# Kernel optimization log

Measured on AMD Instinct MI355X. Metric: run time of the kernel, lower is better.

The kernel has to match this reference:

```python
import jax, jax.numpy as jnp
import numpy as np

B, S, D = 4, 2048, 1152
H, KVH, HD = 16, 4, 64
SW = 1792
NEG = jnp.float32(-1e9)


def setup_inputs() -> dict:
    key = jax.random.key(0)
    ks = jax.random.split(key, 6)
    x = jax.random.normal(ks[0], (B, S, D), jnp.float32)
    s = 0.02
    wq = jax.random.normal(ks[1], (H * HD, D), jnp.float32) * s
    wk = jax.random.normal(ks[2], (KVH * HD, D), jnp.float32) * s
    wv = jax.random.normal(ks[3], (KVH * HD, D), jnp.float32) * s
    wo = jax.random.normal(ks[4], (D, H * HD), jnp.float32) * s
    # rotary freqs: theta=10000, standard llama-style
    inv = 1.0 / (10000.0 ** (np.arange(0, HD, 2, dtype=np.float32) / HD))
    t = np.arange(S, dtype=np.float32)
    fr = np.outer(t, inv)  # [S, HD//2]
    freqs_cos = jnp.asarray(np.cos(fr), jnp.float32)
    freqs_sin = jnp.asarray(np.sin(fr), jnp.float32)
    positions = jnp.arange(S, dtype=jnp.int32)
    # sliding-window causal additive mask: attend j iff 0 <= i-j < SW
    i = jnp.arange(S)[:, None]
    j = jnp.arange(S)[None, :]
    allowed = (j <= i) & (i - j < SW)
    mask = jnp.where(allowed, jnp.float32(0.0), NEG)
    cache_k = jnp.zeros((B, SW, KVH, HD), jnp.float32)
    cache_v = jnp.zeros((B, SW, KVH, HD), jnp.float32)
    return {"x": x, "wq": wq, "wk": wk, "wv": wv, "wo": wo,
            "freqs_cos": freqs_cos, "freqs_sin": freqs_sin, "mask": mask,
            "cache_k": cache_k, "cache_v": cache_v, "positions": positions}


def _rope(t, cos, sin):
    # t: [B,S,h,HD]; complex multiply on (even, odd) pairs
    tr = t.reshape(t.shape[:-1] + (HD // 2, 2))
    a, b = tr[..., 0], tr[..., 1]
    c = cos[None, :, None, :]
    s = sin[None, :, None, :]
    out = jnp.stack([a * c - b * s, a * s + b * c], axis=-1)
    return out.reshape(t.shape)


def reference(x, wq, wk, wv, wo, freqs_cos, freqs_sin, mask, cache_k, cache_v, positions):
    bsz, seqlen, _ = x.shape
    xq = jnp.einsum('bsd,ed->bse', x, wq).reshape(bsz, seqlen, H, HD)
    xk = jnp.einsum('bsd,ed->bse', x, wk).reshape(bsz, seqlen, KVH, HD)
    xv = jnp.einsum('bsd,ed->bse', x, wv).reshape(bsz, seqlen, KVH, HD)
    xq = _rope(xq, freqs_cos, freqs_sin)
    xk = _rope(xk, freqs_cos, freqs_sin)
    # circular-buffer cache scatter (last SW tokens, modulo indexing)
    idx = positions[-SW:] % SW
    new_ck = cache_k.at[:, idx].set(xk[:, -SW:])
    new_cv = cache_v.at[:, idx].set(xv[:, -SW:])
    # GQA: expand kv heads (repeat_interleave on head dim)
    rep = H // KVH
    key = jnp.repeat(xk, rep, axis=2)   # [B,S,H,HD]
    value = jnp.repeat(xv, rep, axis=2)
    q = xq.transpose(0, 2, 1, 3)        # [B,H,S,HD]
    k = key.transpose(0, 2, 1, 3)
    v = value.transpose(0, 2, 1, 3)
    scale = 1.0 / jnp.sqrt(jnp.float32(HD))
    scores = jnp.einsum('bhqd,bhkd->bhqk', q, k) * scale + mask[None, None]
    probs = jax.nn.softmax(scores, axis=-1)
    out = jnp.einsum('bhqk,bhkd->bhqd', probs, v)
    out = out.transpose(0, 2, 1, 3).reshape(bsz, seqlen, H * HD)
    out = jnp.einsum('bse,de->bsd', out, wo)
    return out, new_ck, new_cv
```

## Files before the change

### kernel.cpp

```cpp
#include <hip/hip_runtime.h>
#include <cstdint>
#include <cstddef>


typedef unsigned short u16;
typedef unsigned int   u32;
typedef __attribute__((ext_vector_type(8))) short bf16x8;
typedef __attribute__((ext_vector_type(4))) float f32x4;

#define AS1(p) ((const __attribute__((address_space(1))) void*)(p))
#define AS3(p) ((__attribute__((address_space(3))) void*)(p))

__device__ __forceinline__ u16 f2bf(float f) {
  u32 u = __float_as_uint(f);
  u += 0x7fffu + ((u >> 16) & 1u);
  return (u16)(u >> 16);
}
__device__ __forceinline__ float bf2f(u32 x) { return __uint_as_float(x << 16); }
__device__ __forceinline__ f32x4 mfma16(bf16x8 a, bf16x8 b, f32x4 c) {
  return __builtin_amdgcn_mfma_f32_16x16x32_bf16(a, b, c, 0, 0, 0);
}
__device__ __forceinline__ u32 cvtpk_bf16(float lo, float hi) {
  u32 r;
  asm("v_cvt_pk_bf16_f32 %0, %1, %2" : "=v"(r) : "v"(lo), "v"(hi));
  return r;
}

__global__ __launch_bounds__(256) void cvt5_kernel(const float* __restrict__ x,
                                                   const float* __restrict__ wq,
                                                   const float* __restrict__ wk,
                                                   const float* __restrict__ wv,
                                                   const float* __restrict__ wo,
                                                   u16* __restrict__ xb,
                                                   u16* __restrict__ wqkvb,
                                                   u16* __restrict__ wob) {
  int i = blockIdx.x * 256 + threadIdx.x;
  const float* in; u16* out; int off;
  if (i < 2359296)      { in = x;  out = xb;                  off = i; }
  else if (i < 2654208) { in = wq; out = wqkvb;               off = i - 2359296; }
  else if (i < 2727936) { in = wk; out = wqkvb + 1024 * 1152; off = i - 2654208; }
  else if (i < 2801664) { in = wv; out = wqkvb + 1280 * 1152; off = i - 2727936; }
  else                  { in = wo; out = wob;                 off = i - 2801664; }
  float4 v = ((const float4*)in)[off];
  uint2 o;
  o.x = (u32)f2bf(v.x) | ((u32)f2bf(v.y) << 16);
  o.y = (u32)f2bf(v.z) | ((u32)f2bf(v.w) << 16);
  ((uint2*)out)[off] = o;
}

template<int BF16_OUT>
__global__ __launch_bounds__(256) void gemm_bt(const u16* __restrict__ A,
                                               const u16* __restrict__ B,
                                               void* __restrict__ C,
                                               int M, int N, int K, int NT) {
  __shared__ u16 As[128][64];
  __shared__ u16 Bs[128][64];
  const int tid  = threadIdx.x;
  const int w    = tid >> 6, lane = tid & 63;
  const int l15  = lane & 15, hi4 = lane >> 4;
  const int lid  = blockIdx.x;
  const int k_   = lid >> 3;
  const int by   = (lid & 7) + 8 * (k_ / NT);
  const int bx   = k_ % NT;
  const int m0   = by * 128, n0 = bx * 128;
  const int wr   = w >> 1, wc = w & 1;

  const int srow = lane >> 3;
  const int scol = ((lane & 7) ^ srow) << 3;
  const u16* Ab = A + (size_t)(m0 + w * 32 + srow) * K + scol;
  const u16* Bb = B + (size_t)(n0 + w * 32 + srow) * K + scol;
  u16* AsDst = &As[w * 32][0];
  u16* BsDst = &Bs[w * 32][0];

  const int swz = (l15 & 7) << 4;
  const int c0  = (((hi4 * 16)      ^ swz) >> 1);
  const int c1  = (((64 + hi4 * 16) ^ swz) >> 1);
  const u16* aRd = &As[wr * 64 + l15][0];
  const u16* bRd = &Bs[wc * 64 + l15][0];

  f32x4 acc[4][4] = {};

  for (int kk = 0; kk < K; kk += 64) {
#pragma unroll
    for (int q = 0; q < 4; q++) {
      __builtin_amdgcn_global_load_lds(AS1(Ab + kk + (size_t)q * 8 * K),
                                       AS3(AsDst + q * 8 * 64), 16, 0, 0);
      __builtin_amdgcn_global_load_lds(AS1(Bb + kk + (size_t)q * 8 * K),
                                       AS3(BsDst + q * 8 * 64), 16, 0, 0);
    }
    __syncthreads();
#pragma unroll
    for (int ks = 0; ks < 2; ks++) {
      const int cc = ks ? c1 : c0;
      bf16x8 af[4], bfr[4];
#pragma unroll
      for (int t = 0; t < 4; t++) af[t]  = *(const bf16x8*)(aRd + t * 16 * 64 + cc);
#pragma unroll
      for (int t = 0; t < 4; t++) bfr[t] = *(const bf16x8*)(bRd + t * 16 * 64 + cc);
#pragma unroll
      for (int mi = 0; mi < 4; mi++)
#pragma unroll
        for (int ni = 0; ni < 4; ni++)
          acc[mi][ni] = mfma16(af[mi], bfr[ni], acc[mi][ni]);
    }
    __syncthreads();
  }

#pragma unroll
  for (int mi = 0; mi < 4; mi++) {
#pragma unroll
    for (int r = 0; r < 4; r++) {
      int row = m0 + wr * 64 + mi * 16 + hi4 * 4 + r;
      size_t base = (size_t)row * N + n0 + wc * 64 + l15;
#pragma unroll
      for (int ni = 0; ni < 4; ni++) {
        float v = acc[mi][ni][r];
        if (BF16_OUT) ((u16*)C)[base + ni * 16] = f2bf(v);
        else          ((float*)C)[base + ni * 16] = v;
      }
    }
  }
}

__global__ __launch_bounds__(256) void ropev_kernel(u16* __restrict__ buf,
                                                    float* __restrict__ kcache,
                                                    u16* __restrict__ vT,
                                                    float* __restrict__ ncv,
                                                    const float* __restrict__ cosT,
                                                    const float* __restrict__ sinT) {
  __shared__ u16 tile[64][65];
  if (blockIdx.x < 20480) {
    int idx = blockIdx.x * 256 + threadIdx.x;
    const bool isQ = idx < 4194304;
    int pi = isQ ? idx : idx - 4194304;
    int m  = isQ ? (pi >> 9) : (pi >> 7);
    int p  = isQ ? (pi & 511) : (pi & 127);
    int coloff = isQ ? 0 : 512;
    int s = m & 2047, b = m >> 11;
    int hh = p & 31;
    u32* bp = (u32*)buf + (size_t)m * 768 + coloff + p;
    u32 pk = *bp;
    float a  = bf2f(pk & 0xffffu), bb = bf2f(pk >> 16);
    float c  = cosT[s * 32 + hh],  sn = sinT[s * 32 + hh];
    float o0 = a * c - bb * sn;
    float o1 = a * sn + bb * c;
    const float qs = isQ ? 0.18033688011112042f : 1.0f;
    *bp = (u32)f2bf(o0 * qs) | ((u32)f2bf(o1 * qs) << 16);
    if (!isQ && s >= 256) {
      int pc = (s < 1792) ? s : s - 1792;
      float2* cp = (float2*)(kcache + (size_t)(b * 1792 + pc) * 256 + 2 * p);
      *cp = make_float2(o0, o1);
    }
  } else {
    int bi = blockIdx.x - 20480;
    int s0 = (bi & 31) * 64, kvh = (bi >> 5) & 3, b = bi >> 7;
    int t = threadIdx.x;
    int r = t >> 2, cc = (t & 3) * 16;
    const u16* src = buf + (size_t)(b * 2048 + s0 + r) * 1536 + 1280 + kvh * 64 + cc;
    uint4 v0 = *(const uint4*)src;
    uint4 v1 = *(const uint4*)(src + 8);
    u16 vals[16];
    *(uint4*)&vals[0] = v0;
    *(uint4*)&vals[8] = v1;
    int s = s0 + r;
    if (s >= 256) {
      int pc = (s < 1792) ? s : s - 1792;
      float* dst = ncv + (size_t)(b * 1792 + pc) * 256 + kvh * 64 + cc;
#pragma unroll
      for (int i = 0; i < 16; i += 4) {
        float4 f = make_float4(bf2f(vals[i]), bf2f(vals[i + 1]),
                               bf2f(vals[i + 2]), bf2f(vals[i + 3]));
        *(float4*)(dst + i) = f;
      }
    }
#pragma unroll
    for (int i = 0; i < 16; i++) tile[cc + i][r] = vals[i];
    __syncthreads();
    u16 ov[16];
#pragma unroll
    for (int i = 0; i < 16; i++) ov[i] = tile[r][cc + i];
    u16* dst2 = vT + (size_t)((b * 4 + kvh) * 64 + r) * 2048 + s0 + cc;
    *(uint4*)dst2 = *(uint4*)&ov[0];
    *(uint4*)(dst2 + 8) = *(uint4*)&ov[8];
  }
}

__global__ __launch_bounds__(256) void attn_kernel(const u16* __restrict__ qkv,
                                                   const u16* __restrict__ vT,
                                                   u16* __restrict__ attnb) {
  __shared__ __align__(16) u16 Kbuf[2][64][64];
  __shared__ __align__(16) u16 Vbuf[2][64][64];
  const int tid = threadIdx.x;
  const int w = tid >> 6, lane = tid & 63;
  const int l15 = lane & 15, hi4 = lane >> 4;

  const int lid  = blockIdx.x;
  const int wgid = (lid & 7) * 128 + (lid >> 3);
  const int gx   = wgid & 63;
  const int rr   = wgid >> 6;
  const int kvh  = rr & 3, b = rr >> 2;
  const int i0   = 32 * (63 - gx);
  const int h    = kvh * 4 + w;

  const u16* qbase = qkv + (size_t)(b * 2048) * 1536 + h * 64;
  const u16* kbase = qkv + (size_t)(b * 2048) * 1536 + 1024 + kvh * 64;
  const u16* vbase = vT + (size_t)((b * 4 + kvh) * 64) * 2048;

  bf16x8 qa[2][2];
  {
    const u16* qp = qbase + (size_t)(i0 + l15) * 1536 + hi4 * 8;
#pragma unroll
    for (int m = 0; m < 2; m++)
#pragma unroll
      for (int ki = 0; ki < 2; ki++)
        qa[m][ki] = *(const bf16x8*)(qp + m * 16 * 1536 + ki * 32);
  }

  bf16x8 ones;
#pragma unroll
  for (int i = 0; i < 8; i++) ones[i] = (short)0x3F80;

  f32x4 o[2][4] = {};
  f32x4 ol[2] = {};

  const int srow = lane >> 3;
  const int ssl  = (lane & 7) ^ srow;

#define STAGE(J0, BS)                                                                     \
  do {                                                                                    \
    _Pragma("unroll")                                                                     \
    for (int q = 0; q < 2; q++) {                                                         \
      const int row = 32 * q + 8 * w + srow;                                              \
      __builtin_amdgcn_global_load_lds(AS1(kbase + (size_t)((J0) + row) * 1536 + ssl * 8),\
                                       AS3(&Kbuf[BS][32 * q + 8 * w][0]), 16, 0, 0);      \
      __builtin_amdgcn_global_load_lds(AS1(vbase + (size_t)row * 2048 + (J0) + ssl * 8),  \
                                       AS3(&Vbuf[BS][32 * q + 8 * w][0]), 16, 0, 0);      \
    }                                                                                     \
  } while (0)

  int jstart = i0 - 1791;
  if (jstart < 0) jstart = 0;
  jstart &= ~63;
  const int jend = i0 + 32;
  const int ntiles = (jend - jstart + 63) >> 6;

  STAGE(jstart, 0);
  if (ntiles > 1) STAGE(jstart + 64, 1);

  for (int t = 0; t < ntiles; t++) {
    const int j0 = jstart + 64 * t;
    if (t + 1 < ntiles) asm volatile("s_waitcnt vmcnt(4)" ::: "memory");
    else                asm volatile("s_waitcnt vmcnt(0)" ::: "memory");
    __builtin_amdgcn_s_barrier();
    __builtin_amdgcn_sched_barrier(0);

    const u16* Kb = &Kbuf[t & 1][0][0];
    const u16* Vb = &Vbuf[t & 1][0][0];

    bf16x8 kf[2][4];
#pragma unroll
    for (int nt = 0; nt < 4; nt++)
#pragma unroll
      for (int ki = 0; ki < 2; ki++)
        kf[ki][nt] = *(const bf16x8*)(Kb + (nt * 16 + l15) * 64 +
                                      (((ki * 4 + hi4) ^ (l15 & 7)) << 3));

    u32 vfd[4][2][4];
#pragma unroll
    for (int tt = 0; tt < 4; tt++) {
      const int row = tt * 16 + l15;
      const u16* Vrow = Vb + row * 64;
      const int rs = row & 7;
      const int inner = (hi4 & 1) * 4;
      const int h1 = hi4 >> 1;
#pragma unroll
      for (int kbp = 0; kbp < 2; kbp++) {
        int us0 = (((4 * kbp + h1)     ^ rs) << 3) + inner;
        int us1 = (((4 * kbp + 2 + h1) ^ rs) << 3) + inner;
        uint2 lo = *(const uint2*)(Vrow + us0);
        uint2 hi = *(const uint2*)(Vrow + us1);
        vfd[tt][kbp][0] = lo.x; vfd[tt][kbp][1] = lo.y;
        vfd[tt][kbp][2] = hi.x; vfd[tt][kbp][3] = hi.y;
      }
    }
    asm volatile("s_waitcnt lgkmcnt(0)" ::: "memory");
    __builtin_amdgcn_sched_barrier(0);
    __builtin_amdgcn_s_barrier();
    if (t + 2 < ntiles) STAGE(j0 + 128, t & 1);

    __builtin_amdgcn_s_setprio(1);
    const bool fast = (j0 + 63 <= i0) && (i0 + 31 - j0 < 1792);
#pragma unroll
    for (int m = 0; m < 2; m++) {
      __align__(16) u32 pkb[8];
#pragma unroll
      for (int nt = 0; nt < 4; nt++) {
        f32x4 s = {0.f, 0.f, 0.f, 0.f};
        s = mfma16(kf[0][nt], qa[m][0], s);
        s = mfma16(kf[1][nt], qa[m][1], s);
        float p[4];
        if (fast) {
#pragma unroll
          for (int r = 0; r < 4; r++) p[r] = __builtin_amdgcn_exp2f(s[r]);
        } else {
#pragma unroll
          for (int r = 0; r < 4; r++) {
            const int j = j0 + nt * 16 + hi4 * 4 + r;
            const int i = i0 + m * 16 + l15;
            p[r] = (j <= i && i - j < 1792) ? __builtin_amdgcn_exp2f(s[r]) : 0.f;
          }
        }
        pkb[nt * 2]     = cvtpk_bf16(p[0], p[1]);
        pkb[nt * 2 + 1] = cvtpk_bf16(p[2], p[3]);
      }
      bf16x8 pa0 = *(const bf16x8*)&pkb[0];
      bf16x8 pa1 = *(const bf16x8*)&pkb[4];
#pragma unroll
      for (int tt = 0; tt < 4; tt++) {
        o[m][tt] = mfma16(pa0, *(const bf16x8*)&vfd[tt][0][0], o[m][tt]);
        o[m][tt] = mfma16(pa1, *(const bf16x8*)&vfd[tt][1][0], o[m][tt]);
      }
      ol[m] = mfma16(pa0, ones, ol[m]);
      ol[m] = mfma16(pa1, ones, ol[m]);
    }
    __builtin_amdgcn_s_setprio(0);
  }
#undef STAGE

  u16* op = attnb + (size_t)(b * 2048 + i0 + hi4 * 4) * 1024 + h * 64 + l15;
#pragma unroll
  for (int m = 0; m < 2; m++)
#pragma unroll
    for (int r = 0; r < 4; r++) {
      float inv = 1.0f / ol[m][r];
#pragma unroll
      for (int tt = 0; tt < 4; tt++)
        op[(size_t)(m * 16 + r) * 1024 + 16 * tt] = f2bf(o[m][tt][r] * inv);
    }
}

extern "C" void kernel_launch(void* const* d_in, const int* in_sizes, int n_in,
                              void* d_out, int out_size, void* d_ws, size_t ws_size,
                              hipStream_t stream) {
  const float* x  = (const float*)d_in[0];
  const float* wq = (const float*)d_in[1];
  const float* wk = (const float*)d_in[2];
  const float* wv = (const float*)d_in[3];
  const float* wo = (const float*)d_in[4];
  const float* fc = (const float*)d_in[5];
  const float* fs = (const float*)d_in[6];

  float* out = (float*)d_out;
  float* nck = out + 9437184;
  float* ncv = nck + 1835008;

  char* ws = (char*)d_ws;
  u16* attnb = (u16*)(ws);
  u16* xb    = (u16*)(ws);
  u16* wqkvb = (u16*)(ws + 18874368);
  u16* wob   = (u16*)(ws + 22413312);
  u16* qkv   = (u16*)(ws + 24772608);
  u16* vT    = (u16*)(ws + 49938432);

  cvt5_kernel<<<12096, 256, 0, stream>>>(x, wq, wk, wv, wo, xb, wqkvb, wob);

  gemm_bt<1><<<768, 256, 0, stream>>>(xb, wqkvb, qkv, 8192, 1536, 1152, 12);

  ropev_kernel<<<20992, 256, 0, stream>>>(qkv, nck, vT, ncv, fc, fs);

  attn_kernel<<<1024, 256, 0, stream>>>(qkv, vT, attnb);

  gemm_bt<0><<<576, 256, 0, stream>>>(attnb, wob, out, 8192, 1152, 1024, 9);
}
```

Measured before the change: 161.3 us.

## Fuse Q rotary into attention Q load and fold softmax scale into Wq

Q rope is now applied in registers when the attention kernel loads its Q fragments, and the softmax scale is folded into the bf16 conversion of Wq. The separate rope kernel only processes K and the V transpose, which removes a full read-modify-write pass over Q. The attention workgroup-to-tile mapping is also changed to interleave long and short causal rows for load balance. Applying the scale before rounding slightly changes bf16 rounding.

```diff
diff --git a/kernel.cpp b/kernel.cpp
--- a/kernel.cpp
+++ b/kernel.cpp
@@ -35,16 +35,17 @@
                                                    u16* __restrict__ wqkvb,
                                                    u16* __restrict__ wob) {
   int i = blockIdx.x * 256 + threadIdx.x;
-  const float* in; u16* out; int off;
+  const float* in; u16* out; int off; float sc = 1.0f;
   if (i < 2359296)      { in = x;  out = xb;                  off = i; }
-  else if (i < 2654208) { in = wq; out = wqkvb;               off = i - 2359296; }
+  else if (i < 2654208) { in = wq; out = wqkvb;               off = i - 2359296;
+                          sc = 0.18033688011112042f; }
   else if (i < 2727936) { in = wk; out = wqkvb + 1024 * 1152; off = i - 2654208; }
   else if (i < 2801664) { in = wv; out = wqkvb + 1280 * 1152; off = i - 2727936; }
   else                  { in = wo; out = wob;                 off = i - 2801664; }
   float4 v = ((const float4*)in)[off];
   uint2 o;
-  o.x = (u32)f2bf(v.x) | ((u32)f2bf(v.y) << 16);
-  o.y = (u32)f2bf(v.z) | ((u32)f2bf(v.w) << 16);
+  o.x = (u32)f2bf(v.x * sc) | ((u32)f2bf(v.y * sc) << 16);
+  o.y = (u32)f2bf(v.z * sc) | ((u32)f2bf(v.w * sc) << 16);
   ((uint2*)out)[off] = o;
 }
 
@@ -129,30 +130,25 @@
                                                     const float* __restrict__ cosT,
                                                     const float* __restrict__ sinT) {
   __shared__ u16 tile[64][65];
-  if (blockIdx.x < 20480) {
+  if (blockIdx.x < 4096) {
     int idx = blockIdx.x * 256 + threadIdx.x;
-    const bool isQ = idx < 4194304;
-    int pi = isQ ? idx : idx - 4194304;
-    int m  = isQ ? (pi >> 9) : (pi >> 7);
-    int p  = isQ ? (pi & 511) : (pi & 127);
-    int coloff = isQ ? 0 : 512;
+    int m = idx >> 7, p = idx & 127;
     int s = m & 2047, b = m >> 11;
     int hh = p & 31;
-    u32* bp = (u32*)buf + (size_t)m * 768 + coloff + p;
+    u32* bp = (u32*)buf + (size_t)m * 768 + 512 + p;
     u32 pk = *bp;
     float a  = bf2f(pk & 0xffffu), bb = bf2f(pk >> 16);
     float c  = cosT[s * 32 + hh],  sn = sinT[s * 32 + hh];
     float o0 = a * c - bb * sn;
     float o1 = a * sn + bb * c;
-    const float qs = isQ ? 0.18033688011112042f : 1.0f;
-    *bp = (u32)f2bf(o0 * qs) | ((u32)f2bf(o1 * qs) << 16);
-    if (!isQ && s >= 256) {
+    *bp = (u32)f2bf(o0) | ((u32)f2bf(o1) << 16);
+    if (s >= 256) {
       int pc = (s < 1792) ? s : s - 1792;
       float2* cp = (float2*)(kcache + (size_t)(b * 1792 + pc) * 256 + 2 * p);
       *cp = make_float2(o0, o1);
     }
   } else {
-    int bi = blockIdx.x - 20480;
+    int bi = blockIdx.x - 4096;
     int s0 = (bi & 31) * 64, kvh = (bi >> 5) & 3, b = bi >> 7;
     int t = threadIdx.x;
     int r = t >> 2, cc = (t & 3) * 16;
@@ -187,20 +183,24 @@
 
 __global__ __launch_bounds__(256) void attn_kernel(const u16* __restrict__ qkv,
                                                    const u16* __restrict__ vT,
-                                                   u16* __restrict__ attnb) {
+                                                   u16* __restrict__ attnb,
+                                                   const float* __restrict__ cosT,
+                                                   const float* __restrict__ sinT) {
   __shared__ __align__(16) u16 Kbuf[2][64][64];
   __shared__ __align__(16) u16 Vbuf[2][64][64];
   const int tid = threadIdx.x;
   const int w = tid >> 6, lane = tid & 63;
   const int l15 = lane & 15, hi4 = lane >> 4;
 
-  const int lid  = blockIdx.x;
-  const int wgid = (lid & 7) * 128 + (lid >> 3);
-  const int gx   = wgid & 63;
-  const int rr   = wgid >> 6;
-  const int kvh  = rr & 3, b = rr >> 2;
-  const int i0   = 32 * (63 - gx);
-  const int h    = kvh * 4 + w;
+  const int lid = blockIdx.x;
+  const int g   = lid & 7;
+  const int t_  = lid >> 3;
+  const int u_  = t_ >> 1, v_ = t_ & 1;
+  const int c   = v_ ? u_ : (63 - u_);
+  const int rr  = 2 * g + v_;
+  const int kvh = rr & 3, b = rr >> 2;
+  const int i0  = 32 * c;
+  const int h   = kvh * 4 + w;
 
   const u16* qbase = qkv + (size_t)(b * 2048) * 1536 + h * 64;
   const u16* kbase = qkv + (size_t)(b * 2048) * 1536 + 1024 + kvh * 64;
@@ -210,10 +210,34 @@
   {
     const u16* qp = qbase + (size_t)(i0 + l15) * 1536 + hi4 * 8;
 #pragma unroll
-    for (int m = 0; m < 2; m++)
-#pragma unroll
-      for (int ki = 0; ki < 2; ki++)
-        qa[m][ki] = *(const bf16x8*)(qp + m * 16 * 1536 + ki * 32);
+    for (int m = 0; m < 2; m++) {
+      const int s = i0 + m * 16 + l15;
+#pragma unroll
+      for (int ki = 0; ki < 2; ki++) {
+        bf16x8 qv = *(const bf16x8*)(qp + m * 16 * 1536 + ki * 32);
+        const int hh0 = ki * 16 + hi4 * 4;
+        float4 cs = *(const float4*)(cosT + s * 32 + hh0);
+        float4 sn = *(const float4*)(sinT + s * 32 + hh0);
+        u32 wds[4];
+        {
+          float a = bf2f((u16)qv[0]), bb2 = bf2f((u16)qv[1]);
+          wds[0] = cvtpk_bf16(a * cs.x - bb2 * sn.x, a * sn.x + bb2 * cs.x);
+        }
+        {
+          float a = bf2f((u16)qv[2]), bb2 = bf2f((u16)qv[3]);
+          wds[1] = cvtpk_bf16(a * cs.y - bb2 * sn.y, a * sn.y + bb2 * cs.y);
+        }
+        {
+          float a = bf2f((u16)qv[4]), bb2 = bf2f((u16)qv[5]);
+          wds[2] = cvtpk_bf16(a * cs.z - bb2 * sn.z, a * sn.z + bb2 * cs.z);
+        }
+        {
+          float a = bf2f((u16)qv[6]), bb2 = bf2f((u16)qv[7]);
+          wds[3] = cvtpk_bf16(a * cs.w - bb2 * sn.w, a * sn.w + bb2 * cs.w);
+        }
+        qa[m][ki] = *(const bf16x8*)&wds[0];
+      }
+    }
   }
 
   bf16x8 ones;
@@ -366,9 +390,9 @@
 
   gemm_bt<1><<<768, 256, 0, stream>>>(xb, wqkvb, qkv, 8192, 1536, 1152, 12);
 
-  ropev_kernel<<<20992, 256, 0, stream>>>(qkv, nck, vT, ncv, fc, fs);
-
-  attn_kernel<<<1024, 256, 0, stream>>>(qkv, vT, attnb);
+  ropev_kernel<<<4608, 256, 0, stream>>>(qkv, nck, vT, ncv, fc, fs);
+
+  attn_kernel<<<1024, 256, 0, stream>>>(qkv, vT, attnb, fc, fs);
 
   gemm_bt<0><<<576, 256, 0, stream>>>(attnb, wob, out, 8192, 1152, 1024, 9);
 }
```

Result: slower. 183.8 us (+14.0%).

## Split long attention query tiles across two workgroups and merge partial results

Applied to the files above, without the earlier changes.

Query tiles in rows 1536-2047, which have the longest key ranges, are now split into two halves along the key dimension and handled by separate workgroups. Each half writes unnormalized fp32 partial outputs and row sums to workspace, and a new merge kernel adds them and normalizes. The grid grows from 1024 to 1280 blocks and is reordered to balance per-XCD load and shorten the tail. The cost is an extra kernel launch plus fp32 partial-result traffic. Summing un-rescaled partials is valid only because the kernel uses no running max.

```diff
diff --git a/kernel.cpp b/kernel.cpp
--- a/kernel.cpp
+++ b/kernel.cpp
@@ -187,20 +187,28 @@
 
 __global__ __launch_bounds__(256) void attn_kernel(const u16* __restrict__ qkv,
                                                    const u16* __restrict__ vT,
-                                                   u16* __restrict__ attnb) {
+                                                   u16* __restrict__ attnb,
+                                                   float* __restrict__ Opart,
+                                                   float* __restrict__ lpart) {
   __shared__ __align__(16) u16 Kbuf[2][64][64];
   __shared__ __align__(16) u16 Vbuf[2][64][64];
   const int tid = threadIdx.x;
   const int w = tid >> 6, lane = tid & 63;
   const int l15 = lane & 15, hi4 = lane >> 4;
 
-  const int lid  = blockIdx.x;
-  const int wgid = (lid & 7) * 128 + (lid >> 3);
-  const int gx   = wgid & 63;
-  const int rr   = wgid >> 6;
-  const int kvh  = rr & 3, b = rr >> 2;
-  const int i0   = 32 * (63 - gx);
-  const int h    = kvh * 4 + w;
+  const int lid   = blockIdx.x;
+  const int xcd   = lid & 7;
+  const int t_    = lid >> 3;
+  const int panel = (t_ >= 80) ? 1 : 0;
+  const int seq   = t_ - 80 * panel;
+  int c, half = 0, split = 0;
+  if (seq < 24)      { c = 47 - seq; }
+  else if (seq < 56) { int ci = seq - 24; c = 63 - (ci >> 1); half = ci & 1; split = 1; }
+  else               { c = 79 - seq; }
+  const int rr  = 2 * xcd + panel;
+  const int kvh = rr & 3, b = rr >> 2;
+  const int i0  = 32 * c;
+  const int h   = kvh * 4 + w;
 
   const u16* qbase = qkv + (size_t)(b * 2048) * 1536 + h * 64;
   const u16* kbase = qkv + (size_t)(b * 2048) * 1536 + 1024 + kvh * 64;
@@ -241,16 +249,21 @@
   int jstart = i0 - 1791;
   if (jstart < 0) jstart = 0;
   jstart &= ~63;
-  const int jend = i0 + 32;
-  const int ntiles = (jend - jstart + 63) >> 6;
-
-  STAGE(jstart, 0);
-  if (ntiles > 1) STAGE(jstart + 64, 1);
-
-  for (int t = 0; t < ntiles; t++) {
-    const int j0 = jstart + 64 * t;
-    if (t + 1 < ntiles) asm volatile("s_waitcnt vmcnt(4)" ::: "memory");
-    else                asm volatile("s_waitcnt vmcnt(0)" ::: "memory");
+  const int T = (i0 + 32 - jstart + 63) >> 6;
+  int js = jstart, ntc = T;
+  if (split) {
+    const int nF = (T + 1) >> 1;
+    if (half == 0) { ntc = nF; }
+    else           { js = jstart + 64 * nF; ntc = T - nF; }
+  }
+
+  STAGE(js, 0);
+  if (ntc > 1) STAGE(js + 64, 1);
+
+  for (int t = 0; t < ntc; t++) {
+    const int j0 = js + 64 * t;
+    if (t + 1 < ntc) asm volatile("s_waitcnt vmcnt(4)" ::: "memory");
+    else             asm volatile("s_waitcnt vmcnt(0)" ::: "memory");
     __builtin_amdgcn_s_barrier();
     __builtin_amdgcn_sched_barrier(0);
 
@@ -286,7 +299,7 @@
     asm volatile("s_waitcnt lgkmcnt(0)" ::: "memory");
     __builtin_amdgcn_sched_barrier(0);
     __builtin_amdgcn_s_barrier();
-    if (t + 2 < ntiles) STAGE(j0 + 128, t & 1);
+    if (t + 2 < ntc) STAGE(j0 + 128, t & 1);
 
     __builtin_amdgcn_s_setprio(1);
     const bool fast = (j0 + 63 <= i0) && (i0 + 31 - j0 < 1792);
@@ -327,16 +340,58 @@
   }
 #undef STAGE
 
-  u16* op = attnb + (size_t)(b * 2048 + i0 + hi4 * 4) * 1024 + h * 64 + l15;
-#pragma unroll
-  for (int m = 0; m < 2; m++)
-#pragma unroll
-    for (int r = 0; r < 4; r++) {
-      float inv = 1.0f / ol[m][r];
-#pragma unroll
-      for (int tt = 0; tt < 4; tt++)
-        op[(size_t)(m * 16 + r) * 1024 + 16 * tt] = f2bf(o[m][tt][r] * inv);
-    }
+  if (!split) {
+    u16* op = attnb + (size_t)(b * 2048 + i0 + hi4 * 4) * 1024 + h * 64 + l15;
+#pragma unroll
+    for (int m = 0; m < 2; m++)
+#pragma unroll
+      for (int r = 0; r < 4; r++) {
+        float inv = 1.0f / ol[m][r];
+#pragma unroll
+        for (int tt = 0; tt < 4; tt++)
+          op[(size_t)(m * 16 + r) * 1024 + 16 * tt] = f2bf(o[m][tt][r] * inv);
+      }
+  } else {
+    float* Ob = Opart + ((size_t)(half * 4 + b) * 512 + (i0 - 1536) + hi4 * 4) * 1024
+                + h * 64 + l15;
+#pragma unroll
+    for (int m = 0; m < 2; m++)
+#pragma unroll
+      for (int r = 0; r < 4; r++) {
+        float* Or = Ob + (size_t)(m * 16 + r) * 1024;
+#pragma unroll
+        for (int tt = 0; tt < 4; tt++) Or[16 * tt] = o[m][tt][r];
+      }
+    if (l15 == 0) {
+#pragma unroll
+      for (int m = 0; m < 2; m++)
+#pragma unroll
+        for (int r = 0; r < 4; r++)
+          lpart[((size_t)(half * 4 + b) * 512 + (i0 - 1536) + m * 16 + hi4 * 4 + r) * 16 + h]
+            = ol[m][r];
+    }
+  }
+}
+
+__global__ __launch_bounds__(256) void attn_merge(const float* __restrict__ Opart,
+                                                  const float* __restrict__ lpart,
+                                                  u16* __restrict__ attnb) {
+  int gid = blockIdx.x * 256 + threadIdx.x;
+  int col4 = gid & 255;
+  int rg = gid >> 8;
+  int b = rg >> 9, row = rg & 511;
+  int h = col4 >> 4;
+  size_t base0 = ((size_t)(0 * 4 + b) * 512 + row) * 1024 + col4 * 4;
+  size_t base1 = ((size_t)(1 * 4 + b) * 512 + row) * 1024 + col4 * 4;
+  float4 a = *(const float4*)(Opart + base0);
+  float4 c2 = *(const float4*)(Opart + base1);
+  float l = lpart[((size_t)(0 * 4 + b) * 512 + row) * 16 + h]
+          + lpart[((size_t)(1 * 4 + b) * 512 + row) * 16 + h];
+  float inv = 1.0f / l;
+  uint2 o;
+  o.x = (u32)f2bf((a.x + c2.x) * inv) | ((u32)f2bf((a.y + c2.y) * inv) << 16);
+  o.y = (u32)f2bf((a.z + c2.z) * inv) | ((u32)f2bf((a.w + c2.w) * inv) << 16);
+  *(uint2*)(attnb + (size_t)(b * 2048 + 1536 + row) * 1024 + col4 * 4) = o;
 }
 
 extern "C" void kernel_launch(void* const* d_in, const int* in_sizes, int n_in,
@@ -355,12 +410,14 @@
   float* ncv = nck + 1835008;
 
   char* ws = (char*)d_ws;
-  u16* attnb = (u16*)(ws);
-  u16* xb    = (u16*)(ws);
-  u16* wqkvb = (u16*)(ws + 18874368);
-  u16* wob   = (u16*)(ws + 22413312);
-  u16* qkv   = (u16*)(ws + 24772608);
-  u16* vT    = (u16*)(ws + 49938432);
+  u16*   attnb = (u16*)(ws);
+  u16*   xb    = (u16*)(ws);
+  u16*   wqkvb = (u16*)(ws + 18874368);
+  u16*   wob   = (u16*)(ws + 22413312);
+  u16*   qkv   = (u16*)(ws + 24772608);
+  u16*   vT    = (u16*)(ws + 49938432);
+  float* Opart = (float*)(ws + 54132736);
+  float* lpart = (float*)(ws + 70909952);
 
   cvt5_kernel<<<12096, 256, 0, stream>>>(x, wq, wk, wv, wo, xb, wqkvb, wob);
 
@@ -368,7 +425,9 @@
 
   ropev_kernel<<<20992, 256, 0, stream>>>(qkv, nck, vT, ncv, fc, fs);
 
-  attn_kernel<<<1024, 256, 0, stream>>>(qkv, vT, attnb);
+  attn_kernel<<<1280, 256, 0, stream>>>(qkv, vT, attnb, Opart, lpart);
+
+  attn_merge<<<2048, 256, 0, stream>>>(Opart, lpart, attnb);
 
   gemm_bt<0><<<576, 256, 0, stream>>>(attnb, wob, out, 8192, 1152, 1024, 9);
 }
```

New measurement: 172.4 us. +6.9%, slower.
